# Kernel tuning notes

Measured on AMD Instinct MI355X. Metric: run time of the kernel, lower is better.

The kernel has to match this reference:

```python
import jax, jax.numpy as jnp
import numpy as np

B, L, D = 4, 1024, 256
N_PER, N_HYP = 48, 16  # n_oscillators=64, n_hyperbolic=16
K = N_PER + N_HYP


def _mlp(x, w1, b1, w2, b2):
    # torch nn.Linear: y = x @ W.T + b; GELU is exact (erf) by default
    h = jax.nn.gelu(x @ w1.T + b1, approximate=False)
    return h @ w2.T + b2


def setup_inputs() -> dict:
    key = jax.random.key(0)
    ks = iter(jax.random.split(key, 32))

    def lin(o, i):
        return jax.random.normal(next(ks), (o, i), jnp.float32) * 0.02

    def bias(o):
        return jnp.zeros((o,), jnp.float32)

    inp = {"x": jax.random.normal(next(ks), (B, L, D), jnp.float32)}
    # key/query periodic phase MLPs: Linear(D,D) -> GELU -> Linear(D,N_PER)
    inp.update(kp_w1=lin(D, D), kp_b1=bias(D), kp_w2=lin(N_PER, D), kp_b2=bias(N_PER))
    inp.update(qp_w1=lin(D, D), qp_b1=bias(D), qp_w2=lin(N_PER, D), qp_b2=bias(N_PER))
    # key/query hyperbolic MLPs: Linear(D,D) -> GELU -> Linear(D, 2*N_HYP)
    inp.update(kh_w1=lin(D, D), kh_b1=bias(D), kh_w2=lin(2 * N_HYP, D), kh_b2=bias(2 * N_HYP))
    inp.update(qh_w1=lin(D, D), qh_b1=bias(D), qh_w2=lin(2 * N_HYP, D), qh_b2=bias(2 * N_HYP))
    # value projection and output (LayerNorm + Linear)
    inp.update(v_w=lin(D, D), v_b=bias(D))
    inp.update(ln_g=jnp.ones((D,), jnp.float32), ln_b=jnp.zeros((D,), jnp.float32))
    inp.update(out_w=lin(D, D), out_b=bias(D))
    return inp


def reference(x, kp_w1, kp_b1, kp_w2, kp_b2, qp_w1, qp_b1, qp_w2, qp_b2,
              kh_w1, kh_b1, kh_w2, kh_b2, qh_w1, qh_b1, qh_w2, qh_b2,
              v_w, v_b, ln_g, ln_b, out_w, out_b):
    Bx, Lx, Dx = x.shape

    # periodic (flat torus) phasors: unit-magnitude
    key_p = jnp.tanh(_mlp(x, kp_w1, kp_b1, kp_w2, kp_b2)) * jnp.pi   # (B,L,N_PER)
    query_p = jnp.tanh(_mlp(x, qp_w1, qp_b1, qp_w2, qp_b2)) * jnp.pi
    key_phasor_p = jnp.exp(1j * key_p.astype(jnp.complex64))
    query_phasor_p = jnp.exp(1j * query_p.astype(jnp.complex64))

    # hyperbolic (Poincare-disk) phasors: amplitude = 1 - |z|
    key_h = jnp.tanh(_mlp(x, kh_w1, kh_b1, kh_w2, kh_b2)).reshape(Bx, Lx, N_HYP, 2) * 0.9
    query_h = jnp.tanh(_mlp(x, qh_w1, qh_b1, qh_w2, qh_b2)).reshape(Bx, Lx, N_HYP, 2) * 0.9
    key_ang = jnp.arctan2(key_h[..., 1], key_h[..., 0])
    query_ang = jnp.arctan2(query_h[..., 1], query_h[..., 0])
    key_amp = 1.0 - jnp.sqrt(jnp.sum(key_h * key_h, axis=-1))
    query_amp = 1.0 - jnp.sqrt(jnp.sum(query_h * query_h, axis=-1))
    key_phasor_h = key_amp * jnp.exp(1j * key_ang.astype(jnp.complex64))
    query_phasor_h = query_amp * jnp.exp(1j * query_ang.astype(jnp.complex64))

    key_phasor = jnp.concatenate([key_phasor_p, key_phasor_h], axis=-1)    # (B,L,K)
    query_phasor = jnp.concatenate([query_phasor_p, query_phasor_h], axis=-1)

    V = (x @ v_w.T + v_b).astype(jnp.complex64)                            # (B,L,D)

    # bind: outer product per timestep, cumsum over L (linear-attention scan)
    bound = key_phasor[..., :, None] * V[..., None, :]                     # (B,L,K,D) complex
    memory = jnp.cumsum(bound, axis=1)
    retrieved = jnp.real(jnp.sum(memory * jnp.conj(query_phasor)[..., None], axis=2))  # (B,L,D)

    positions = jnp.arange(1, Lx + 1, dtype=jnp.float32)
    norm = jnp.sqrt(positions * float(K))[None, :, None]
    r = retrieved / norm

    # to_out: LayerNorm(D) -> Linear(D,D)
    mu = jnp.mean(r, axis=-1, keepdims=True)
    var = jnp.mean(jnp.square(r - mu), axis=-1, keepdims=True)
    r_ln = (r - mu) / jnp.sqrt(var + 1e-5) * ln_g + ln_b
    return x + (r_ln @ out_w.T + out_b)
```

## Files before the change

kernel.cpp:

```cpp
#include <hip/hip_runtime.h>
#include <math.h>


#define Bn 4
#define Ln 1024
#define BLn 4096

typedef __attribute__((ext_vector_type(8))) short bf16x8;
typedef __attribute__((ext_vector_type(4))) float f32x4;

__device__ inline float bf2f(ushort u) {
  union { uint u32; float f; } x; x.u32 = ((uint)u) << 16; return x.f;
}
__device__ inline ushort f2bf(float f) {
  union { float f; uint u; } x; x.f = f;
  uint r = x.u + 0x7fffu + ((x.u >> 16) & 1u);
  return (ushort)(r >> 16);
}

struct CastArgs { const float* src[11]; ushort* dst[11]; int rows[11]; int nreal[11]; };

__global__ void cast_bf16(CastArgs a) {
  const int s = blockIdx.y;
  const float* src = a.src[s];
  ushort* dst = a.dst[s];
  const int n = a.rows[s] * 256;
  const int nreal = a.nreal[s];
  for (int i = blockIdx.x * blockDim.x + threadIdx.x; i < n; i += gridDim.x * blockDim.x) {
    int row = i >> 8;
    float v = (row < nreal) ? src[row * 256 + (i & 255)] : 0.f;
    dst[i] = f2bf(v);
  }
}

struct MProb { const ushort* X; const ushort* W; const float* bias; const float* res;
               void* Y; int act; int Nreal; float scale; int ldY; };
struct MArgs { MProb p[5]; };

__global__ __launch_bounds__(256) void gemm_mfma(MArgs args) {
  const MProb p = args.p[blockIdx.z];
  __shared__ ushort As[64 * 40];
  __shared__ ushort Bs[64 * 40];
  const int tid = threadIdx.x;
  const int m0 = blockIdx.x * 64, n0 = blockIdx.y * 64;
  const int lane = tid & 63, wave = tid >> 6;
  const int wr = wave >> 1, wc = wave & 1;
  const int fr = lane & 15, quad = lane >> 4;
  f32x4 acc[2][2];
#pragma unroll
  for (int i = 0; i < 2; i++)
#pragma unroll
    for (int j = 0; j < 2; j++) acc[i][j] = (f32x4){0.f, 0.f, 0.f, 0.f};

  const int srow = tid >> 2, sch = (tid & 3) * 8;
  for (int k0 = 0; k0 < 256; k0 += 32) {
    uint4 va = *(const uint4*)(p.X + (size_t)(m0 + srow) * 256 + k0 + sch);
    uint4 vb = *(const uint4*)(p.W + (size_t)(n0 + srow) * 256 + k0 + sch);
    *(uint4*)&As[srow * 40 + sch] = va;
    *(uint4*)&Bs[srow * 40 + sch] = vb;
    __syncthreads();
    bf16x8 a0 = *(const bf16x8*)&As[(wr * 32 + fr) * 40 + quad * 8];
    bf16x8 a1 = *(const bf16x8*)&As[(wr * 32 + 16 + fr) * 40 + quad * 8];
    bf16x8 b0 = *(const bf16x8*)&Bs[(wc * 32 + fr) * 40 + quad * 8];
    bf16x8 b1 = *(const bf16x8*)&Bs[(wc * 32 + 16 + fr) * 40 + quad * 8];
    acc[0][0] = __builtin_amdgcn_mfma_f32_16x16x32_bf16(a0, b0, acc[0][0], 0, 0, 0);
    acc[0][1] = __builtin_amdgcn_mfma_f32_16x16x32_bf16(a0, b1, acc[0][1], 0, 0, 0);
    acc[1][0] = __builtin_amdgcn_mfma_f32_16x16x32_bf16(a1, b0, acc[1][0], 0, 0, 0);
    acc[1][1] = __builtin_amdgcn_mfma_f32_16x16x32_bf16(a1, b1, acc[1][1], 0, 0, 0);
    __syncthreads();
  }
#pragma unroll
  for (int i = 0; i < 2; i++)
#pragma unroll
    for (int j = 0; j < 2; j++) {
      int col = n0 + wc * 32 + j * 16 + fr;
      float bv = (col < p.Nreal) ? p.bias[col] : 0.f;
      if (p.act == 4) {
        ushort4 st;
        int rowg0 = m0 + wr * 32 + i * 16 + quad * 4;
        st.x = f2bf(acc[i][j][0] + bv);
        st.y = f2bf(acc[i][j][1] + bv);
        st.z = f2bf(acc[i][j][2] + bv);
        st.w = f2bf(acc[i][j][3] + bv);
        *(ushort4*)((ushort*)p.Y + (size_t)col * 4096 + rowg0) = st;
      } else {
#pragma unroll
        for (int r = 0; r < 4; r++) {
          int rowg = m0 + wr * 32 + i * 16 + quad * 4 + r;
          float o = acc[i][j][r] + bv;
          if (p.act == 1) o = 0.5f * o * (1.0f + erff(o * 0.70710678118654752f));
          else if (p.act == 2) o = tanhf(o) * p.scale;
          else if (p.act == 3) o += p.res[(size_t)rowg * 256 + col];
          if (p.act == 1) ((ushort*)p.Y)[(size_t)rowg * p.ldY + col] = f2bf(o);
          else ((float*)p.Y)[(size_t)rowg * p.ldY + col] = o;
        }
      }
    }
}

__global__ __launch_bounds__(256) void phasor_t(const float* kp, const float* qp,
                                                const float* kh, const float* qh,
                                                uint* PhiQ, uint* PhiK, uint* PhiKT) {
  __shared__ ushort LK[64][130];
  const int t = threadIdx.x;
  const int row0 = blockIdx.x * 64;
  const int b = row0 >> 10;
  const int lb0 = row0 & 1023;
#pragma unroll
  for (int it = 0; it < 16; it++) {
    int idx = t + it * 256;
    int k = idx & 63, rl = idx >> 6;
    int row = row0 + rl;
    float kre, kim, qre, qim;
    if (k < 48) {
      float ka = kp[row * 64 + k], qa = qp[row * 64 + k];
      __sincosf(ka, &kim, &kre);
      __sincosf(qa, &qim, &qre);
    } else {
      int j2 = (k - 48) * 2;
      float av = kh[row * 64 + j2], bv = kh[row * 64 + j2 + 1];
      float rr = sqrtf(av * av + bv * bv);
      if (rr > 0.f) { float inv = (1.0f - rr) / rr; kre = av * inv; kim = bv * inv; }
      else          { kre = 1.0f; kim = 0.0f; }
      av = qh[row * 64 + j2]; bv = qh[row * 64 + j2 + 1];
      rr = sqrtf(av * av + bv * bv);
      if (rr > 0.f) { float inv = (1.0f - rr) / rr; qre = av * inv; qim = bv * inv; }
      else          { qre = 1.0f; qim = 0.0f; }
    }
    uint pk = (uint)f2bf(kre) | ((uint)f2bf(kim) << 16);
    uint pq = (uint)f2bf(qre) | ((uint)f2bf(qim) << 16);
    PhiK[(size_t)row * 64 + k] = pk;
    PhiQ[(size_t)row * 64 + k] = pq;
    *(uint*)&LK[rl][2 * k] = pk;
  }
  __syncthreads();
#pragma unroll
  for (int it = 0; it < 16; it++) {
    int idx = t + it * 256;
    int k2 = idx >> 5, lp = idx & 31;
    uint v = (uint)LK[lp * 2][k2] | ((uint)LK[lp * 2 + 1][k2] << 16);
    PhiKT[(size_t)b * 65536 + k2 * 512 + (lb0 >> 1) + lp] = v;
  }
}

__global__ __launch_bounds__(256) void kv_chunk(const ushort* VT, const ushort* PhiKT,
                                                float* P) {
  const int bc = blockIdx.x;
  const int b = bc >> 4, c = bc & 15;
  const int d0 = blockIdx.y * 128;
  const int tid = threadIdx.x, lane = tid & 63, wave = tid >> 6;
  const int wr = wave >> 1, wc = wave & 1;
  const int fr = lane & 15, quad = lane >> 4;
  const int colb = b * 1024 + c * 64;
  f32x4 acc[4][4];
#pragma unroll
  for (int i = 0; i < 4; i++)
#pragma unroll
    for (int j = 0; j < 4; j++) acc[i][j] = (f32x4){0.f, 0.f, 0.f, 0.f};
#pragma unroll
  for (int kk = 0; kk < 2; kk++) {
    bf16x8 a[4], bb[4];
#pragma unroll
    for (int i = 0; i < 4; i++)
      a[i] = *(const bf16x8*)(VT + (size_t)(d0 + wr * 64 + i * 16 + fr) * 4096 + colb + kk * 32 + quad * 8);
#pragma unroll
    for (int j = 0; j < 4; j++)
      bb[j] = *(const bf16x8*)(PhiKT + (size_t)b * 131072 + (size_t)(wc * 64 + j * 16 + fr) * 1024 + c * 64 + kk * 32 + quad * 8);
#pragma unroll
    for (int i = 0; i < 4; i++)
#pragma unroll
      for (int j = 0; j < 4; j++)
        acc[i][j] = __builtin_amdgcn_mfma_f32_16x16x32_bf16(a[i], bb[j], acc[i][j], 0, 0, 0);
  }
#pragma unroll
  for (int i = 0; i < 4; i++)
#pragma unroll
    for (int j = 0; j < 4; j++)
#pragma unroll
      for (int r = 0; r < 4; r++) {
        int d = d0 + wr * 64 + i * 16 + quad * 4 + r;
        int k2 = wc * 64 + j * 16 + fr;
        P[((size_t)bc * 256 + d) * 128 + k2] = acc[i][j][r];
      }
}

__global__ void prefix_scan(const float* P, ushort* SpreB) {
  int gid = blockIdx.x * 256 + threadIdx.x;
  int b = gid >> 15, dk = gid & 32767;
  size_t idx = (size_t)b * 16 * 32768 + dk;
  float run = 0.f;
#pragma unroll 4
  for (int c = 0; c < 16; c++) {
    SpreB[idx] = f2bf(run);
    run += P[idx];
    idx += 32768;
  }
}

__global__ __launch_bounds__(256) void retrieve(const ushort* PhiQ, const ushort* PhiK,
                                                const ushort* VT, const ushort* SpreB,
                                                float* R) {
  __shared__ ushort Sl[64 * 72];
  const int bc = blockIdx.x;
  const int b = bc >> 4, c = bc & 15;
  const int d0 = blockIdx.y * 128;
  const int tid = threadIdx.x, lane = tid & 63, wy = tid >> 6;
  const int fr = lane & 15, quad = lane >> 4;
  const int g0 = b * 1024 + c * 64;
  bf16x8 a[4][4];
#pragma unroll
  for (int i = 0; i < 4; i++)
#pragma unroll
    for (int kk = 0; kk < 4; kk++)
      a[i][kk] = *(const bf16x8*)(PhiQ + (size_t)(g0 + i * 16 + fr) * 128 + kk * 32 + quad * 8);

  f32x4 acc[4][2];
#pragma unroll
  for (int i = 0; i < 4; i++)
#pragma unroll
    for (int j = 0; j < 2; j++) acc[i][j] = (f32x4){0.f, 0.f, 0.f, 0.f};

#pragma unroll
  for (int kk = 0; kk < 4; kk++) {
    bf16x8 bb[2];
#pragma unroll
    for (int j = 0; j < 2; j++)
      bb[j] = *(const bf16x8*)(SpreB + ((size_t)bc * 256 + d0 + wy * 32 + j * 16 + fr) * 128 + kk * 32 + quad * 8);
#pragma unroll
    for (int i = 0; i < 4; i++)
#pragma unroll
      for (int j = 0; j < 2; j++)
        acc[i][j] = __builtin_amdgcn_mfma_f32_16x16x32_bf16(a[i][kk], bb[j], acc[i][j], 0, 0, 0);
  }

  f32x4 sacc[4];
#pragma unroll
  for (int i = 0; i < 4; i++) sacc[i] = (f32x4){0.f, 0.f, 0.f, 0.f};
#pragma unroll
  for (int kk = 0; kk < 4; kk++) {
    bf16x8 bs = *(const bf16x8*)(PhiK + (size_t)(g0 + wy * 16 + fr) * 128 + kk * 32 + quad * 8);
#pragma unroll
    for (int i = 0; i < 4; i++)
      sacc[i] = __builtin_amdgcn_mfma_f32_16x16x32_bf16(a[i][kk], bs, sacc[i], 0, 0, 0);
  }
#pragma unroll
  for (int i = 0; i < 4; i++)
#pragma unroll
    for (int r = 0; r < 4; r++) {
      int row = i * 16 + quad * 4 + r;
      int col = wy * 16 + fr;
      Sl[row * 72 + col] = (col <= row) ? f2bf(sacc[i][r]) : (ushort)0;
    }
  __syncthreads();

#pragma unroll
  for (int kk = 0; kk < 2; kk++) {
    bf16x8 as[4], bv[2];
#pragma unroll
    for (int i = 0; i < 4; i++)
      as[i] = *(const bf16x8*)&Sl[(i * 16 + fr) * 72 + kk * 32 + quad * 8];
#pragma unroll
    for (int j = 0; j < 2; j++)
      bv[j] = *(const bf16x8*)(VT + (size_t)(d0 + wy * 32 + j * 16 + fr) * 4096 + g0 + kk * 32 + quad * 8);
#pragma unroll
    for (int i = 0; i < 4; i++)
#pragma unroll
      for (int j = 0; j < 2; j++)
        acc[i][j] = __builtin_amdgcn_mfma_f32_16x16x32_bf16(as[i], bv[j], acc[i][j], 0, 0, 0);
  }

#pragma unroll
  for (int i = 0; i < 4; i++)
#pragma unroll
    for (int j = 0; j < 2; j++)
#pragma unroll
      for (int r = 0; r < 4; r++) {
        int row = i * 16 + quad * 4 + r;
        int d = d0 + wy * 32 + j * 16 + fr;
        float scale = rsqrtf((float)((c * 64 + row + 1) * 64));
        R[(size_t)(g0 + row) * 256 + d] = acc[i][j][r] * scale;
      }
}

__global__ __launch_bounds__(256) void layernorm(const float* Rin, const float* g,
                                                 const float* bta, ushort* Y) {
  __shared__ float red[8];
  const int row = blockIdx.x;
  const int tid = threadIdx.x;
  float v = Rin[(size_t)row * 256 + tid];
  float s = v, sq = v * v;
#pragma unroll
  for (int off = 32; off >= 1; off >>= 1) {
    s  += __shfl_down(s, off, 64);
    sq += __shfl_down(sq, off, 64);
  }
  int wave = tid >> 6;
  if ((tid & 63) == 0) { red[wave * 2] = s; red[wave * 2 + 1] = sq; }
  __syncthreads();
  float ts = 0.f, tsq = 0.f;
#pragma unroll
  for (int w = 0; w < 4; w++) { ts += red[w * 2]; tsq += red[w * 2 + 1]; }
  float mean = ts * (1.0f / 256.0f);
  float var = fmaxf(tsq * (1.0f / 256.0f) - mean * mean, 0.f);
  float rstd = rsqrtf(var + 1e-5f);
  Y[(size_t)row * 256 + tid] = f2bf((v - mean) * rstd * g[tid] + bta[tid]);
}

extern "C" void kernel_launch(void* const* d_in, const int* in_sizes, int n_in,
                              void* d_out, int out_size, void* d_ws, size_t ws_size,
                              hipStream_t stream) {
  const float* x     = (const float*)d_in[0];
  const float* kp_w1 = (const float*)d_in[1];
  const float* kp_b1 = (const float*)d_in[2];
  const float* kp_w2 = (const float*)d_in[3];
  const float* kp_b2 = (const float*)d_in[4];
  const float* qp_w1 = (const float*)d_in[5];
  const float* qp_b1 = (const float*)d_in[6];
  const float* qp_w2 = (const float*)d_in[7];
  const float* qp_b2 = (const float*)d_in[8];
  const float* kh_w1 = (const float*)d_in[9];
  const float* kh_b1 = (const float*)d_in[10];
  const float* kh_w2 = (const float*)d_in[11];
  const float* kh_b2 = (const float*)d_in[12];
  const float* qh_w1 = (const float*)d_in[13];
  const float* qh_b1 = (const float*)d_in[14];
  const float* qh_w2 = (const float*)d_in[15];
  const float* qh_b2 = (const float*)d_in[16];
  const float* v_w   = (const float*)d_in[17];
  const float* v_b   = (const float*)d_in[18];
  const float* ln_g  = (const float*)d_in[19];
  const float* ln_b  = (const float*)d_in[20];
  const float* out_w = (const float*)d_in[21];
  const float* out_b = (const float*)d_in[22];

  char* ws = (char*)d_ws;
  const size_t MiB = 1024 * 1024;
  ushort* xb   = (ushort*)(ws + 0);
  ushort* wb1[6];
  for (int i = 0; i < 6; i++) wb1[i] = (ushort*)(ws + 2 * MiB + (size_t)i * 256 * 1024);
  ushort* wb2[4];
  for (int i = 0; i < 4; i++) wb2[i] = (ushort*)(ws + 3 * MiB + 512 * 1024 + (size_t)i * 64 * 1024);
  ushort* h0   = (ushort*)(ws + 4 * MiB);
  ushort* h1   = (ushort*)(ws + 6 * MiB);
  ushort* h2   = (ushort*)(ws + 8 * MiB);
  ushort* h3   = (ushort*)(ws + 10 * MiB);
  ushort* VT   = (ushort*)(ws + 12 * MiB);
  float*  kp   = (float*)(ws + 14 * MiB);
  float*  qp   = (float*)(ws + 15 * MiB);
  float*  kh   = (float*)(ws + 16 * MiB);
  float*  qh   = (float*)(ws + 17 * MiB);
  uint*   PhiQ = (uint*)(ws + 18 * MiB);
  uint*   PhiK = (uint*)(ws + 19 * MiB);
  uint*   PhiKT= (uint*)(ws + 20 * MiB);
  ushort* SpreB= (ushort*)(ws + 21 * MiB);
  float*  P    = (float*)(ws + 25 * MiB);
  float*  r    = (float*)(ws + 33 * MiB);
  ushort* rln  = (ushort*)(ws + 37 * MiB);

  CastArgs ca;
  const float* srcs[11] = { x, kp_w1, qp_w1, kh_w1, qh_w1, v_w, out_w,
                            kp_w2, qp_w2, kh_w2, qh_w2 };
  ushort* dsts[11] = { xb, wb1[0], wb1[1], wb1[2], wb1[3], wb1[4], wb1[5],
                       wb2[0], wb2[1], wb2[2], wb2[3] };
  int rows[11]  = { 4096, 256, 256, 256, 256, 256, 256, 64, 64, 64, 64 };
  int nreal[11] = { 4096, 256, 256, 256, 256, 256, 256, 48, 48, 32, 32 };
  for (int i = 0; i < 11; i++) { ca.src[i] = srcs[i]; ca.dst[i] = dsts[i]; ca.rows[i] = rows[i]; ca.nreal[i] = nreal[i]; }
  cast_bf16<<<dim3(256, 11), 256, 0, stream>>>(ca);

  const float PI_F = 3.14159265358979323846f;
  MArgs g1;
  g1.p[0] = { xb, wb1[0], kp_b1, nullptr, h0, 1, 256, 0.f, 256 };
  g1.p[1] = { xb, wb1[1], qp_b1, nullptr, h1, 1, 256, 0.f, 256 };
  g1.p[2] = { xb, wb1[2], kh_b1, nullptr, h2, 1, 256, 0.f, 256 };
  g1.p[3] = { xb, wb1[3], qh_b1, nullptr, h3, 1, 256, 0.f, 256 };
  g1.p[4] = { xb, wb1[4], v_b,   nullptr, VT, 4, 256, 0.f, 0 };
  gemm_mfma<<<dim3(64, 4, 5), 256, 0, stream>>>(g1);

  MArgs g2;
  g2.p[0] = { h0, wb2[0], kp_b2, nullptr, kp, 2, 48, PI_F, 64 };
  g2.p[1] = { h1, wb2[1], qp_b2, nullptr, qp, 2, 48, PI_F, 64 };
  g2.p[2] = { h2, wb2[2], kh_b2, nullptr, kh, 2, 32, 0.9f, 64 };
  g2.p[3] = { h3, wb2[3], qh_b2, nullptr, qh, 2, 32, 0.9f, 64 };
  g2.p[4] = g2.p[0];
  gemm_mfma<<<dim3(64, 1, 4), 256, 0, stream>>>(g2);

  phasor_t<<<dim3(64), 256, 0, stream>>>(kp, qp, kh, qh, PhiQ, PhiK, PhiKT);

  kv_chunk<<<dim3(64, 2), 256, 0, stream>>>(VT, (const ushort*)PhiKT, P);

  prefix_scan<<<dim3(512), 256, 0, stream>>>(P, SpreB);

  retrieve<<<dim3(64, 2), 256, 0, stream>>>((const ushort*)PhiQ, (const ushort*)PhiK,
                                            VT, SpreB, r);

  layernorm<<<dim3(BLn), 256, 0, stream>>>(r, ln_g, ln_b, rln);

  MArgs g3;
  g3.p[0] = { rln, wb1[5], out_b, x, d_out, 3, 256, 0.f, 256 };
  g3.p[1] = g3.p[0]; g3.p[2] = g3.p[0]; g3.p[3] = g3.p[0]; g3.p[4] = g3.p[0];
  gemm_mfma<<<dim3(64, 4, 1), 256, 0, stream>>>(g3);
}
```

Baseline: 177.3 us.

## Fuse pipeline into four kernels: inline casts, GEMM2+phasor, scan+retrieve, LN+out GEMM

Drops the separate bf16 cast kernel by converting fp32 inputs to bf16 while staging GEMM tiles. The second MLP GEMM, tanh and phasor generation now share one kernel, with outputs kept in LDS. The chunk-state computation, prefix scan and retrieval merge into one kernel in which each block recomputes the sum over earlier chunks directly. LayerNorm is folded into the output GEMM. This cuts launches and intermediate HBM traffic, but adds redundant work: scan cost grows with chunk index, causing imbalance across blocks, and weights are reconverted per tile.

```diff
diff --git a/kernel.cpp b/kernel.cpp
--- a/kernel.cpp
+++ b/kernel.cpp
@@ -9,36 +9,20 @@
 typedef __attribute__((ext_vector_type(8))) short bf16x8;
 typedef __attribute__((ext_vector_type(4))) float f32x4;
 
-__device__ inline float bf2f(ushort u) {
-  union { uint u32; float f; } x; x.u32 = ((uint)u) << 16; return x.f;
-}
 __device__ inline ushort f2bf(float f) {
   union { float f; uint u; } x; x.f = f;
   uint r = x.u + 0x7fffu + ((x.u >> 16) & 1u);
   return (ushort)(r >> 16);
 }
-
-struct CastArgs { const float* src[11]; ushort* dst[11]; int rows[11]; int nreal[11]; };
-
-__global__ void cast_bf16(CastArgs a) {
-  const int s = blockIdx.y;
-  const float* src = a.src[s];
-  ushort* dst = a.dst[s];
-  const int n = a.rows[s] * 256;
-  const int nreal = a.nreal[s];
-  for (int i = blockIdx.x * blockDim.x + threadIdx.x; i < n; i += gridDim.x * blockDim.x) {
-    int row = i >> 8;
-    float v = (row < nreal) ? src[row * 256 + (i & 255)] : 0.f;
-    dst[i] = f2bf(v);
-  }
-}
-
-struct MProb { const ushort* X; const ushort* W; const float* bias; const float* res;
-               void* Y; int act; int Nreal; float scale; int ldY; };
-struct MArgs { MProb p[5]; };
-
-__global__ __launch_bounds__(256) void gemm_mfma(MArgs args) {
-  const MProb p = args.p[blockIdx.z];
+__device__ inline uint pk2(float a, float b) {
+  return (uint)f2bf(a) | ((uint)f2bf(b) << 16);
+}
+
+struct G1Prob { const float* X; const float* W; const float* bias; void* Y; int act; };
+struct G1Args { G1Prob p[5]; };
+
+__global__ __launch_bounds__(256) void gemm1(G1Args args) {
+  const G1Prob p = args.p[blockIdx.z];
   __shared__ ushort As[64 * 40];
   __shared__ ushort Bs[64 * 40];
   const int tid = threadIdx.x;
@@ -54,19 +38,23 @@
 
   const int srow = tid >> 2, sch = (tid & 3) * 8;
   for (int k0 = 0; k0 < 256; k0 += 32) {
-    uint4 va = *(const uint4*)(p.X + (size_t)(m0 + srow) * 256 + k0 + sch);
-    uint4 vb = *(const uint4*)(p.W + (size_t)(n0 + srow) * 256 + k0 + sch);
-    *(uint4*)&As[srow * 40 + sch] = va;
-    *(uint4*)&Bs[srow * 40 + sch] = vb;
+    float4 a0 = *(const float4*)(p.X + (size_t)(m0 + srow) * 256 + k0 + sch);
+    float4 a1 = *(const float4*)(p.X + (size_t)(m0 + srow) * 256 + k0 + sch + 4);
+    float4 b0 = *(const float4*)(p.W + (size_t)(n0 + srow) * 256 + k0 + sch);
+    float4 b1 = *(const float4*)(p.W + (size_t)(n0 + srow) * 256 + k0 + sch + 4);
+    uint4 pa = { pk2(a0.x, a0.y), pk2(a0.z, a0.w), pk2(a1.x, a1.y), pk2(a1.z, a1.w) };
+    uint4 pb = { pk2(b0.x, b0.y), pk2(b0.z, b0.w), pk2(b1.x, b1.y), pk2(b1.z, b1.w) };
+    *(uint4*)&As[srow * 40 + sch] = pa;
+    *(uint4*)&Bs[srow * 40 + sch] = pb;
     __syncthreads();
-    bf16x8 a0 = *(const bf16x8*)&As[(wr * 32 + fr) * 40 + quad * 8];
-    bf16x8 a1 = *(const bf16x8*)&As[(wr * 32 + 16 + fr) * 40 + quad * 8];
-    bf16x8 b0 = *(const bf16x8*)&Bs[(wc * 32 + fr) * 40 + quad * 8];
-    bf16x8 b1 = *(const bf16x8*)&Bs[(wc * 32 + 16 + fr) * 40 + quad * 8];
-    acc[0][0] = __builtin_amdgcn_mfma_f32_16x16x32_bf16(a0, b0, acc[0][0], 0, 0, 0);
-    acc[0][1] = __builtin_amdgcn_mfma_f32_16x16x32_bf16(a0, b1, acc[0][1], 0, 0, 0);
-    acc[1][0] = __builtin_amdgcn_mfma_f32_16x16x32_bf16(a1, b0, acc[1][0], 0, 0, 0);
-    acc[1][1] = __builtin_amdgcn_mfma_f32_16x16x32_bf16(a1, b1, acc[1][1], 0, 0, 0);
+    bf16x8 fa0 = *(const bf16x8*)&As[(wr * 32 + fr) * 40 + quad * 8];
+    bf16x8 fa1 = *(const bf16x8*)&As[(wr * 32 + 16 + fr) * 40 + quad * 8];
+    bf16x8 fb0 = *(const bf16x8*)&Bs[(wc * 32 + fr) * 40 + quad * 8];
+    bf16x8 fb1 = *(const bf16x8*)&Bs[(wc * 32 + 16 + fr) * 40 + quad * 8];
+    acc[0][0] = __builtin_amdgcn_mfma_f32_16x16x32_bf16(fa0, fb0, acc[0][0], 0, 0, 0);
+    acc[0][1] = __builtin_amdgcn_mfma_f32_16x16x32_bf16(fa0, fb1, acc[0][1], 0, 0, 0);
+    acc[1][0] = __builtin_amdgcn_mfma_f32_16x16x32_bf16(fa1, fb0, acc[1][0], 0, 0, 0);
+    acc[1][1] = __builtin_amdgcn_mfma_f32_16x16x32_bf16(fa1, fb1, acc[1][1], 0, 0, 0);
     __syncthreads();
   }
 #pragma unroll
@@ -74,10 +62,10 @@
 #pragma unroll
     for (int j = 0; j < 2; j++) {
       int col = n0 + wc * 32 + j * 16 + fr;
-      float bv = (col < p.Nreal) ? p.bias[col] : 0.f;
+      float bv = p.bias[col];
       if (p.act == 4) {
+        int rowg0 = m0 + wr * 32 + i * 16 + quad * 4;
         ushort4 st;
-        int rowg0 = m0 + wr * 32 + i * 16 + quad * 4;
         st.x = f2bf(acc[i][j][0] + bv);
         st.y = f2bf(acc[i][j][1] + bv);
         st.z = f2bf(acc[i][j][2] + bv);
@@ -88,131 +76,167 @@
         for (int r = 0; r < 4; r++) {
           int rowg = m0 + wr * 32 + i * 16 + quad * 4 + r;
           float o = acc[i][j][r] + bv;
-          if (p.act == 1) o = 0.5f * o * (1.0f + erff(o * 0.70710678118654752f));
-          else if (p.act == 2) o = tanhf(o) * p.scale;
-          else if (p.act == 3) o += p.res[(size_t)rowg * 256 + col];
-          if (p.act == 1) ((ushort*)p.Y)[(size_t)rowg * p.ldY + col] = f2bf(o);
-          else ((float*)p.Y)[(size_t)rowg * p.ldY + col] = o;
+          o = 0.5f * o * (1.0f + erff(o * 0.70710678118654752f));
+          ((ushort*)p.Y)[(size_t)rowg * 256 + col] = f2bf(o);
         }
       }
     }
 }
 
-__global__ __launch_bounds__(256) void phasor_t(const float* kp, const float* qp,
-                                                const float* kh, const float* qh,
-                                                uint* PhiQ, uint* PhiK, uint* PhiKT) {
+struct P2Args { const ushort* h[4]; const float* w[4]; const float* bias[4];
+                int Nreal[4]; float scale[4]; uint* PhiQ; uint* PhiK; uint* PhiKT; };
+
+__global__ __launch_bounds__(256) void gemm2_phasor(P2Args a) {
+  __shared__ ushort As[64 * 40];
+  __shared__ ushort Bs[64 * 40];
+  __shared__ float O[4][64][66];
   __shared__ ushort LK[64][130];
-  const int t = threadIdx.x;
+  const int tid = threadIdx.x;
   const int row0 = blockIdx.x * 64;
-  const int b = row0 >> 10;
-  const int lb0 = row0 & 1023;
+  const int b = row0 >> 10, lb0 = row0 & 1023;
+  const int lane = tid & 63, wave = tid >> 6;
+  const int wr = wave >> 1, wc = wave & 1;
+  const int fr = lane & 15, quad = lane >> 4;
+  const int srow = tid >> 2, sch = (tid & 3) * 8;
+
+  for (int pi = 0; pi < 4; pi++) {
+    const ushort* X = a.h[pi];
+    const float* W = a.w[pi];
+    const int Nr = a.Nreal[pi];
+    f32x4 acc[2][2];
+#pragma unroll
+    for (int i = 0; i < 2; i++)
+#pragma unroll
+      for (int j = 0; j < 2; j++) acc[i][j] = (f32x4){0.f, 0.f, 0.f, 0.f};
+    for (int k0 = 0; k0 < 256; k0 += 32) {
+      uint4 pa = *(const uint4*)(X + (size_t)(row0 + srow) * 256 + k0 + sch);
+      float4 b0 = {0.f,0.f,0.f,0.f}, b1 = {0.f,0.f,0.f,0.f};
+      if (srow < Nr) {
+        b0 = *(const float4*)(W + (size_t)srow * 256 + k0 + sch);
+        b1 = *(const float4*)(W + (size_t)srow * 256 + k0 + sch + 4);
+      }
+      uint4 pb = { pk2(b0.x, b0.y), pk2(b0.z, b0.w), pk2(b1.x, b1.y), pk2(b1.z, b1.w) };
+      *(uint4*)&As[srow * 40 + sch] = pa;
+      *(uint4*)&Bs[srow * 40 + sch] = pb;
+      __syncthreads();
+      bf16x8 fa0 = *(const bf16x8*)&As[(wr * 32 + fr) * 40 + quad * 8];
+      bf16x8 fa1 = *(const bf16x8*)&As[(wr * 32 + 16 + fr) * 40 + quad * 8];
+      bf16x8 fb0 = *(const bf16x8*)&Bs[(wc * 32 + fr) * 40 + quad * 8];
+      bf16x8 fb1 = *(const bf16x8*)&Bs[(wc * 32 + 16 + fr) * 40 + quad * 8];
+      acc[0][0] = __builtin_amdgcn_mfma_f32_16x16x32_bf16(fa0, fb0, acc[0][0], 0, 0, 0);
+      acc[0][1] = __builtin_amdgcn_mfma_f32_16x16x32_bf16(fa0, fb1, acc[0][1], 0, 0, 0);
+      acc[1][0] = __builtin_amdgcn_mfma_f32_16x16x32_bf16(fa1, fb0, acc[1][0], 0, 0, 0);
+      acc[1][1] = __builtin_amdgcn_mfma_f32_16x16x32_bf16(fa1, fb1, acc[1][1], 0, 0, 0);
+      __syncthreads();
+    }
+    const float sc = a.scale[pi];
+#pragma unroll
+    for (int i = 0; i < 2; i++)
+#pragma unroll
+      for (int j = 0; j < 2; j++) {
+        int col = wc * 32 + j * 16 + fr;
+        float bv = (col < Nr) ? a.bias[pi][col] : 0.f;
+#pragma unroll
+        for (int r = 0; r < 4; r++) {
+          int row = wr * 32 + i * 16 + quad * 4 + r;
+          O[pi][row][col] = tanhf(acc[i][j][r] + bv) * sc;
+        }
+      }
+  }
+  __syncthreads();
+
 #pragma unroll
   for (int it = 0; it < 16; it++) {
-    int idx = t + it * 256;
+    int idx = tid + it * 256;
     int k = idx & 63, rl = idx >> 6;
     int row = row0 + rl;
     float kre, kim, qre, qim;
     if (k < 48) {
-      float ka = kp[row * 64 + k], qa = qp[row * 64 + k];
+      float ka = O[0][rl][k], qa = O[1][rl][k];
       __sincosf(ka, &kim, &kre);
       __sincosf(qa, &qim, &qre);
     } else {
       int j2 = (k - 48) * 2;
-      float av = kh[row * 64 + j2], bv = kh[row * 64 + j2 + 1];
+      float av = O[2][rl][j2], bv = O[2][rl][j2 + 1];
       float rr = sqrtf(av * av + bv * bv);
       if (rr > 0.f) { float inv = (1.0f - rr) / rr; kre = av * inv; kim = bv * inv; }
       else          { kre = 1.0f; kim = 0.0f; }
-      av = qh[row * 64 + j2]; bv = qh[row * 64 + j2 + 1];
+      av = O[3][rl][j2]; bv = O[3][rl][j2 + 1];
       rr = sqrtf(av * av + bv * bv);
       if (rr > 0.f) { float inv = (1.0f - rr) / rr; qre = av * inv; qim = bv * inv; }
       else          { qre = 1.0f; qim = 0.0f; }
     }
-    uint pk = (uint)f2bf(kre) | ((uint)f2bf(kim) << 16);
-    uint pq = (uint)f2bf(qre) | ((uint)f2bf(qim) << 16);
-    PhiK[(size_t)row * 64 + k] = pk;
-    PhiQ[(size_t)row * 64 + k] = pq;
+    uint pk = pk2(kre, kim);
+    uint pq = pk2(qre, qim);
+    a.PhiK[(size_t)row * 64 + k] = pk;
+    a.PhiQ[(size_t)row * 64 + k] = pq;
     *(uint*)&LK[rl][2 * k] = pk;
   }
   __syncthreads();
 #pragma unroll
   for (int it = 0; it < 16; it++) {
-    int idx = t + it * 256;
+    int idx = tid + it * 256;
     int k2 = idx >> 5, lp = idx & 31;
     uint v = (uint)LK[lp * 2][k2] | ((uint)LK[lp * 2 + 1][k2] << 16);
-    PhiKT[(size_t)b * 65536 + k2 * 512 + (lb0 >> 1) + lp] = v;
-  }
-}
-
-__global__ __launch_bounds__(256) void kv_chunk(const ushort* VT, const ushort* PhiKT,
-                                                float* P) {
+    a.PhiKT[(size_t)b * 65536 + k2 * 512 + (lb0 >> 1) + lp] = v;
+  }
+}
+
+__global__ __launch_bounds__(256) void scan_fused(const ushort* PhiQ, const ushort* PhiK,
+                                                  const ushort* PhiKT, const ushort* VT,
+                                                  float* R) {
+  __shared__ ushort S_lds[128 * 144];
+  __shared__ ushort Sl[64 * 72];
   const int bc = blockIdx.x;
   const int b = bc >> 4, c = bc & 15;
   const int d0 = blockIdx.y * 128;
   const int tid = threadIdx.x, lane = tid & 63, wave = tid >> 6;
   const int wr = wave >> 1, wc = wave & 1;
   const int fr = lane & 15, quad = lane >> 4;
-  const int colb = b * 1024 + c * 64;
-  f32x4 acc[4][4];
-#pragma unroll
-  for (int i = 0; i < 4; i++)
-#pragma unroll
-    for (int j = 0; j < 4; j++) acc[i][j] = (f32x4){0.f, 0.f, 0.f, 0.f};
-#pragma unroll
-  for (int kk = 0; kk < 2; kk++) {
-    bf16x8 a[4], bb[4];
-#pragma unroll
-    for (int i = 0; i < 4; i++)
-      a[i] = *(const bf16x8*)(VT + (size_t)(d0 + wr * 64 + i * 16 + fr) * 4096 + colb + kk * 32 + quad * 8);
+
+  f32x4 st[4][4];
+#pragma unroll
+  for (int i = 0; i < 4; i++)
+#pragma unroll
+    for (int j = 0; j < 4; j++) st[i][j] = (f32x4){0.f, 0.f, 0.f, 0.f};
+  for (int cc = 0; cc < c; cc++) {
+    const int colb = b * 1024 + cc * 64;
+#pragma unroll
+    for (int kk = 0; kk < 2; kk++) {
+      bf16x8 av[4], bv[4];
+#pragma unroll
+      for (int i = 0; i < 4; i++)
+        av[i] = *(const bf16x8*)(VT + (size_t)(d0 + wr * 64 + i * 16 + fr) * 4096 + colb + kk * 32 + quad * 8);
+#pragma unroll
+      for (int j = 0; j < 4; j++)
+        bv[j] = *(const bf16x8*)(PhiKT + (size_t)b * 131072 + (size_t)(wc * 64 + j * 16 + fr) * 1024 + cc * 64 + kk * 32 + quad * 8);
+#pragma unroll
+      for (int i = 0; i < 4; i++)
+#pragma unroll
+        for (int j = 0; j < 4; j++)
+          st[i][j] = __builtin_amdgcn_mfma_f32_16x16x32_bf16(av[i], bv[j], st[i][j], 0, 0, 0);
+    }
+  }
+#pragma unroll
+  for (int i = 0; i < 4; i++)
 #pragma unroll
     for (int j = 0; j < 4; j++)
-      bb[j] = *(const bf16x8*)(PhiKT + (size_t)b * 131072 + (size_t)(wc * 64 + j * 16 + fr) * 1024 + c * 64 + kk * 32 + quad * 8);
-#pragma unroll
-    for (int i = 0; i < 4; i++)
-#pragma unroll
-      for (int j = 0; j < 4; j++)
-        acc[i][j] = __builtin_amdgcn_mfma_f32_16x16x32_bf16(a[i], bb[j], acc[i][j], 0, 0, 0);
-  }
-#pragma unroll
-  for (int i = 0; i < 4; i++)
-#pragma unroll
-    for (int j = 0; j < 4; j++)
 #pragma unroll
       for (int r = 0; r < 4; r++) {
-        int d = d0 + wr * 64 + i * 16 + quad * 4 + r;
+        int dl = wr * 64 + i * 16 + quad * 4 + r;
         int k2 = wc * 64 + j * 16 + fr;
-        P[((size_t)bc * 256 + d) * 128 + k2] = acc[i][j][r];
-      }
-}
-
-__global__ void prefix_scan(const float* P, ushort* SpreB) {
-  int gid = blockIdx.x * 256 + threadIdx.x;
-  int b = gid >> 15, dk = gid & 32767;
-  size_t idx = (size_t)b * 16 * 32768 + dk;
-  float run = 0.f;
-#pragma unroll 4
-  for (int c = 0; c < 16; c++) {
-    SpreB[idx] = f2bf(run);
-    run += P[idx];
-    idx += 32768;
-  }
-}
-
-__global__ __launch_bounds__(256) void retrieve(const ushort* PhiQ, const ushort* PhiK,
-                                                const ushort* VT, const ushort* SpreB,
-                                                float* R) {
-  __shared__ ushort Sl[64 * 72];
-  const int bc = blockIdx.x;
-  const int b = bc >> 4, c = bc & 15;
-  const int d0 = blockIdx.y * 128;
-  const int tid = threadIdx.x, lane = tid & 63, wy = tid >> 6;
-  const int fr = lane & 15, quad = lane >> 4;
+        S_lds[dl * 144 + k2] = f2bf(st[i][j][r]);
+      }
+  __syncthreads();
+
+  const int wy = wave;
   const int g0 = b * 1024 + c * 64;
-  bf16x8 a[4][4];
+  bf16x8 aq[4][4];
 #pragma unroll
   for (int i = 0; i < 4; i++)
 #pragma unroll
     for (int kk = 0; kk < 4; kk++)
-      a[i][kk] = *(const bf16x8*)(PhiQ + (size_t)(g0 + i * 16 + fr) * 128 + kk * 32 + quad * 8);
+      aq[i][kk] = *(const bf16x8*)(PhiQ + (size_t)(g0 + i * 16 + fr) * 128 + kk * 32 + quad * 8);
 
   f32x4 acc[4][2];
 #pragma unroll
@@ -225,12 +249,12 @@
     bf16x8 bb[2];
 #pragma unroll
     for (int j = 0; j < 2; j++)
-      bb[j] = *(const bf16x8*)(SpreB + ((size_t)bc * 256 + d0 + wy * 32 + j * 16 + fr) * 128 + kk * 32 + quad * 8);
+      bb[j] = *(const bf16x8*)&S_lds[(wy * 32 + j * 16 + fr) * 144 + kk * 32 + quad * 8];
 #pragma unroll
     for (int i = 0; i < 4; i++)
 #pragma unroll
       for (int j = 0; j < 2; j++)
-        acc[i][j] = __builtin_amdgcn_mfma_f32_16x16x32_bf16(a[i][kk], bb[j], acc[i][j], 0, 0, 0);
+        acc[i][j] = __builtin_amdgcn_mfma_f32_16x16x32_bf16(aq[i][kk], bb[j], acc[i][j], 0, 0, 0);
   }
 
   f32x4 sacc[4];
@@ -241,7 +265,7 @@
     bf16x8 bs = *(const bf16x8*)(PhiK + (size_t)(g0 + wy * 16 + fr) * 128 + kk * 32 + quad * 8);
 #pragma unroll
     for (int i = 0; i < 4; i++)
-      sacc[i] = __builtin_amdgcn_mfma_f32_16x16x32_bf16(a[i][kk], bs, sacc[i], 0, 0, 0);
+      sacc[i] = __builtin_amdgcn_mfma_f32_16x16x32_bf16(aq[i][kk], bs, sacc[i], 0, 0, 0);
   }
 #pragma unroll
   for (int i = 0; i < 4; i++)
@@ -255,18 +279,18 @@
 
 #pragma unroll
   for (int kk = 0; kk < 2; kk++) {
-    bf16x8 as[4], bv[2];
+    bf16x8 as[4], bvv[2];
 #pragma unroll
     for (int i = 0; i < 4; i++)
       as[i] = *(const bf16x8*)&Sl[(i * 16 + fr) * 72 + kk * 32 + quad * 8];
 #pragma unroll
     for (int j = 0; j < 2; j++)
-      bv[j] = *(const bf16x8*)(VT + (size_t)(d0 + wy * 32 + j * 16 + fr) * 4096 + g0 + kk * 32 + quad * 8);
+      bvv[j] = *(const bf16x8*)(VT + (size_t)(d0 + wy * 32 + j * 16 + fr) * 4096 + g0 + kk * 32 + quad * 8);
 #pragma unroll
     for (int i = 0; i < 4; i++)
 #pragma unroll
       for (int j = 0; j < 2; j++)
-        acc[i][j] = __builtin_amdgcn_mfma_f32_16x16x32_bf16(as[i], bv[j], acc[i][j], 0, 0, 0);
+        acc[i][j] = __builtin_amdgcn_mfma_f32_16x16x32_bf16(as[i], bvv[j], acc[i][j], 0, 0, 0);
   }
 
 #pragma unroll
@@ -282,28 +306,83 @@
       }
 }
 
-__global__ __launch_bounds__(256) void layernorm(const float* Rin, const float* g,
-                                                 const float* bta, ushort* Y) {
-  __shared__ float red[8];
-  const int row = blockIdx.x;
+__global__ __launch_bounds__(256) void out_ln_gemm(const float* r, const float* g,
+                                                   const float* bta, const float* W,
+                                                   const float* ob, const float* x,
+                                                   float* Y) {
+  __shared__ ushort A_lds[64 * 272];
+  __shared__ ushort Bs[64 * 40];
+  __shared__ float gs[256], bs2[256];
   const int tid = threadIdx.x;
-  float v = Rin[(size_t)row * 256 + tid];
-  float s = v, sq = v * v;
-#pragma unroll
-  for (int off = 32; off >= 1; off >>= 1) {
-    s  += __shfl_down(s, off, 64);
-    sq += __shfl_down(sq, off, 64);
-  }
-  int wave = tid >> 6;
-  if ((tid & 63) == 0) { red[wave * 2] = s; red[wave * 2 + 1] = sq; }
-  __syncthreads();
-  float ts = 0.f, tsq = 0.f;
-#pragma unroll
-  for (int w = 0; w < 4; w++) { ts += red[w * 2]; tsq += red[w * 2 + 1]; }
-  float mean = ts * (1.0f / 256.0f);
-  float var = fmaxf(tsq * (1.0f / 256.0f) - mean * mean, 0.f);
+  const int m0 = blockIdx.x * 64, n0 = blockIdx.y * 64;
+  gs[tid] = g[tid];
+  bs2[tid] = bta[tid];
+
+  const int row_l = tid >> 2, seg = (tid & 3) * 64;
+  const float* rr = r + (size_t)(m0 + row_l) * 256 + seg;
+  float s = 0.f, sq = 0.f;
+#pragma unroll
+  for (int i = 0; i < 64; i += 4) {
+    float4 v = *(const float4*)(rr + i);
+    s += v.x + v.y + v.z + v.w;
+    sq += v.x * v.x + v.y * v.y + v.z * v.z + v.w * v.w;
+  }
+  s += __shfl_xor(s, 1); sq += __shfl_xor(sq, 1);
+  s += __shfl_xor(s, 2); sq += __shfl_xor(sq, 2);
+  float mean = s * (1.0f / 256.0f);
+  float var = fmaxf(sq * (1.0f / 256.0f) - mean * mean, 0.f);
   float rstd = rsqrtf(var + 1e-5f);
-  Y[(size_t)row * 256 + tid] = f2bf((v - mean) * rstd * g[tid] + bta[tid]);
+  __syncthreads();
+#pragma unroll
+  for (int i = 0; i < 64; i += 4) {
+    float4 v = *(const float4*)(rr + i);
+    int k = seg + i;
+    ushort4 st;
+    st.x = f2bf((v.x - mean) * rstd * gs[k + 0] + bs2[k + 0]);
+    st.y = f2bf((v.y - mean) * rstd * gs[k + 1] + bs2[k + 1]);
+    st.z = f2bf((v.z - mean) * rstd * gs[k + 2] + bs2[k + 2]);
+    st.w = f2bf((v.w - mean) * rstd * gs[k + 3] + bs2[k + 3]);
+    *(ushort4*)&A_lds[row_l * 272 + k] = st;
+  }
+  __syncthreads();
+
+  const int lane = tid & 63, wave = tid >> 6;
+  const int wr = wave >> 1, wc = wave & 1;
+  const int fr = lane & 15, quad = lane >> 4;
+  const int srow = tid >> 2, sch = (tid & 3) * 8;
+  f32x4 acc[2][2];
+#pragma unroll
+  for (int i = 0; i < 2; i++)
+#pragma unroll
+    for (int j = 0; j < 2; j++) acc[i][j] = (f32x4){0.f, 0.f, 0.f, 0.f};
+  for (int k0 = 0; k0 < 256; k0 += 32) {
+    float4 b0 = *(const float4*)(W + (size_t)(n0 + srow) * 256 + k0 + sch);
+    float4 b1 = *(const float4*)(W + (size_t)(n0 + srow) * 256 + k0 + sch + 4);
+    uint4 pb = { pk2(b0.x, b0.y), pk2(b0.z, b0.w), pk2(b1.x, b1.y), pk2(b1.z, b1.w) };
+    *(uint4*)&Bs[srow * 40 + sch] = pb;
+    __syncthreads();
+    bf16x8 fa0 = *(const bf16x8*)&A_lds[(wr * 32 + fr) * 272 + k0 + quad * 8];
+    bf16x8 fa1 = *(const bf16x8*)&A_lds[(wr * 32 + 16 + fr) * 272 + k0 + quad * 8];
+    bf16x8 fb0 = *(const bf16x8*)&Bs[(wc * 32 + fr) * 40 + quad * 8];
+    bf16x8 fb1 = *(const bf16x8*)&Bs[(wc * 32 + 16 + fr) * 40 + quad * 8];
+    acc[0][0] = __builtin_amdgcn_mfma_f32_16x16x32_bf16(fa0, fb0, acc[0][0], 0, 0, 0);
+    acc[0][1] = __builtin_amdgcn_mfma_f32_16x16x32_bf16(fa0, fb1, acc[0][1], 0, 0, 0);
+    acc[1][0] = __builtin_amdgcn_mfma_f32_16x16x32_bf16(fa1, fb0, acc[1][0], 0, 0, 0);
+    acc[1][1] = __builtin_amdgcn_mfma_f32_16x16x32_bf16(fa1, fb1, acc[1][1], 0, 0, 0);
+    __syncthreads();
+  }
+#pragma unroll
+  for (int i = 0; i < 2; i++)
+#pragma unroll
+    for (int j = 0; j < 2; j++) {
+      int col = n0 + wc * 32 + j * 16 + fr;
+      float bv = ob[col];
+#pragma unroll
+      for (int r = 0; r < 4; r++) {
+        int rowg = m0 + wr * 32 + i * 16 + quad * 4 + r;
+        Y[(size_t)rowg * 256 + col] = acc[i][j][r] + bv + x[(size_t)rowg * 256 + col];
+      }
+    }
 }
 
 extern "C" void kernel_launch(void* const* d_in, const int* in_sizes, int n_in,
@@ -335,68 +414,37 @@
 
   char* ws = (char*)d_ws;
   const size_t MiB = 1024 * 1024;
-  ushort* xb   = (ushort*)(ws + 0);
-  ushort* wb1[6];
-  for (int i = 0; i < 6; i++) wb1[i] = (ushort*)(ws + 2 * MiB + (size_t)i * 256 * 1024);
-  ushort* wb2[4];
-  for (int i = 0; i < 4; i++) wb2[i] = (ushort*)(ws + 3 * MiB + 512 * 1024 + (size_t)i * 64 * 1024);
-  ushort* h0   = (ushort*)(ws + 4 * MiB);
-  ushort* h1   = (ushort*)(ws + 6 * MiB);
-  ushort* h2   = (ushort*)(ws + 8 * MiB);
-  ushort* h3   = (ushort*)(ws + 10 * MiB);
-  ushort* VT   = (ushort*)(ws + 12 * MiB);
-  float*  kp   = (float*)(ws + 14 * MiB);
-  float*  qp   = (float*)(ws + 15 * MiB);
-  float*  kh   = (float*)(ws + 16 * MiB);
-  float*  qh   = (float*)(ws + 17 * MiB);
-  uint*   PhiQ = (uint*)(ws + 18 * MiB);
-  uint*   PhiK = (uint*)(ws + 19 * MiB);
-  uint*   PhiKT= (uint*)(ws + 20 * MiB);
-  ushort* SpreB= (ushort*)(ws + 21 * MiB);
-  float*  P    = (float*)(ws + 25 * MiB);
-  float*  r    = (float*)(ws + 33 * MiB);
-  ushort* rln  = (ushort*)(ws + 37 * MiB);
-
-  CastArgs ca;
-  const float* srcs[11] = { x, kp_w1, qp_w1, kh_w1, qh_w1, v_w, out_w,
-                            kp_w2, qp_w2, kh_w2, qh_w2 };
-  ushort* dsts[11] = { xb, wb1[0], wb1[1], wb1[2], wb1[3], wb1[4], wb1[5],
-                       wb2[0], wb2[1], wb2[2], wb2[3] };
-  int rows[11]  = { 4096, 256, 256, 256, 256, 256, 256, 64, 64, 64, 64 };
-  int nreal[11] = { 4096, 256, 256, 256, 256, 256, 256, 48, 48, 32, 32 };
-  for (int i = 0; i < 11; i++) { ca.src[i] = srcs[i]; ca.dst[i] = dsts[i]; ca.rows[i] = rows[i]; ca.nreal[i] = nreal[i]; }
-  cast_bf16<<<dim3(256, 11), 256, 0, stream>>>(ca);
+  ushort* h0   = (ushort*)(ws + 0);
+  ushort* h1   = (ushort*)(ws + 2 * MiB);
+  ushort* h2   = (ushort*)(ws + 4 * MiB);
+  ushort* h3   = (ushort*)(ws + 6 * MiB);
+  ushort* VT   = (ushort*)(ws + 8 * MiB);
+  uint*   PhiQ = (uint*)(ws + 10 * MiB);
+  uint*   PhiK = (uint*)(ws + 11 * MiB);
+  uint*   PhiKT= (uint*)(ws + 12 * MiB);
+  float*  r    = (float*)(ws + 13 * MiB);
+
+  G1Args g1;
+  g1.p[0] = { x, kp_w1, kp_b1, h0, 1 };
+  g1.p[1] = { x, qp_w1, qp_b1, h1, 1 };
+  g1.p[2] = { x, kh_w1, kh_b1, h2, 1 };
+  g1.p[3] = { x, qh_w1, qh_b1, h3, 1 };
+  g1.p[4] = { x, v_w,   v_b,   VT, 4 };
+  gemm1<<<dim3(64, 4, 5), 256, 0, stream>>>(g1);
 
   const float PI_F = 3.14159265358979323846f;
-  MArgs g1;
-  g1.p[0] = { xb, wb1[0], kp_b1, nullptr, h0, 1, 256, 0.f, 256 };
-  g1.p[1] = { xb, wb1[1], qp_b1, nullptr, h1, 1, 256, 0.f, 256 };
-  g1.p[2] = { xb, wb1[2], kh_b1, nullptr, h2, 1, 256, 0.f, 256 };
-  g1.p[3] = { xb, wb1[3], qh_b1, nullptr, h3, 1, 256, 0.f, 256 };
-  g1.p[4] = { xb, wb1[4], v_b,   nullptr, VT, 4, 256, 0.f, 0 };
-  gemm_mfma<<<dim3(64, 4, 5), 256, 0, stream>>>(g1);
-
-  MArgs g2;
-  g2.p[0] = { h0, wb2[0], kp_b2, nullptr, kp, 2, 48, PI_F, 64 };
-  g2.p[1] = { h1, wb2[1], qp_b2, nullptr, qp, 2, 48, PI_F, 64 };
-  g2.p[2] = { h2, wb2[2], kh_b2, nullptr, kh, 2, 32, 0.9f, 64 };
-  g2.p[3] = { h3, wb2[3], qh_b2, nullptr, qh, 2, 32, 0.9f, 64 };
-  g2.p[4] = g2.p[0];
-  gemm_mfma<<<dim3(64, 1, 4), 256, 0, stream>>>(g2);
-
-  phasor_t<<<dim3(64), 256, 0, stream>>>(kp, qp, kh, qh, PhiQ, PhiK, PhiKT);
-
-  kv_chunk<<<dim3(64, 2), 256, 0, stream>>>(VT, (const ushort*)PhiKT, P);
-
-  prefix_scan<<<dim3(512), 256, 0, stream>>>(P, SpreB);
-
-  retrieve<<<dim3(64, 2), 256, 0, stream>>>((const ushort*)PhiQ, (const ushort*)PhiK,
-                                            VT, SpreB, r);
-
-  layernorm<<<dim3(BLn), 256, 0, stream>>>(r, ln_g, ln_b, rln);
-
-  MArgs g3;
-  g3.p[0] = { rln, wb1[5], out_b, x, d_out, 3, 256, 0.f, 256 };
-  g3.p[1] = g3.p[0]; g3.p[2] = g3.p[0]; g3.p[3] = g3.p[0]; g3.p[4] = g3.p[0];
-  gemm_mfma<<<dim3(64, 4, 1), 256, 0, stream>>>(g3);
-}
+  P2Args p2;
+  p2.h[0] = h0; p2.h[1] = h1; p2.h[2] = h2; p2.h[3] = h3;
+  p2.w[0] = kp_w2; p2.w[1] = qp_w2; p2.w[2] = kh_w2; p2.w[3] = qh_w2;
+  p2.bias[0] = kp_b2; p2.bias[1] = qp_b2; p2.bias[2] = kh_b2; p2.bias[3] = qh_b2;
+  p2.Nreal[0] = 48; p2.Nreal[1] = 48; p2.Nreal[2] = 32; p2.Nreal[3] = 32;
+  p2.scale[0] = PI_F; p2.scale[1] = PI_F; p2.scale[2] = 0.9f; p2.scale[3] = 0.9f;
+  p2.PhiQ = PhiQ; p2.PhiK = PhiK; p2.PhiKT = PhiKT;
+  gemm2_phasor<<<dim3(64), 256, 0, stream>>>(p2);
+
+  scan_fused<<<dim3(64, 2), 256, 0, stream>>>((const ushort*)PhiQ, (const ushort*)PhiK,
+                                              (const ushort*)PhiKT, VT, r);
+
+  out_ln_gemm<<<dim3(64, 4), 256, 0, stream>>>(r, ln_g, ln_b, out_w, out_b, x,
+                                               (float*)d_out);
+}
```

Measured after the change: 197.3 us. +11.3%, slower.
